# Performance work log

Measured on AMD Instinct MI355X. Metric: run time of the kernel, lower is better.

## Reference

```python
import jax, jax.numpy as jnp
import numpy as np

B, S, D = 4, 2048, 2048
H, HD = 16, 128  # n_heads, head_dim; H*HD == D


def setup_inputs() -> dict:
    key = jax.random.key(0)
    ks = jax.random.split(key, 9)
    inp = {
        "q": jax.random.normal(ks[0], (B, S, D), dtype=jnp.float32),
        "k": jax.random.normal(ks[1], (B, S, D), dtype=jnp.float32),
        "v": jax.random.normal(ks[2], (B, S, D), dtype=jnp.float32),
        "attention_mask": jax.random.normal(ks[3], (S, S), dtype=jnp.float32),
        "key_padding_mask": jnp.zeros((B, S), dtype=jnp.float32),
        # torch nn.Linear weights are [out_features, in_features], bias=False
        "wq": jax.random.normal(ks[4], (H * HD, D), dtype=jnp.float32) * (1.0 / np.sqrt(D)),
        "wk": jax.random.normal(ks[5], (H * HD, D), dtype=jnp.float32) * (1.0 / np.sqrt(D)),
        "wv": jax.random.normal(ks[6], (H * HD, D), dtype=jnp.float32) * (1.0 / np.sqrt(D)),
        "wo": jax.random.normal(ks[7], (D, H * HD), dtype=jnp.float32) * (1.0 / np.sqrt(H * HD)),
    }
    return inp


def reference(q, k, v, attention_mask, key_padding_mask, wq, wk, wv, wo):
    # projections: x @ W.T, then split into heads -> [B, H, S, HD]
    def proj_heads(x, w):
        y = jnp.einsum('bsd,ed->bse', x, w)
        return y.reshape(B, S, H, HD).transpose(0, 2, 1, 3)

    qh = proj_heads(q, wq)
    kh = proj_heads(k, wk)
    vh = proj_heads(v, wv)

    scale = 1.0 / jnp.sqrt(jnp.asarray(HD, dtype=qh.dtype))
    scores = jnp.einsum('bhqd,bhkd->bhqk', qh, kh) * scale  # [B,H,S,S]
    scores = scores + attention_mask[None, None, :, :]       # additive 2D mask
    scores = scores + key_padding_mask[:, None, None, :]     # additive padding mask
    weights = jax.nn.softmax(scores, axis=-1)
    attn = jnp.einsum('bhqk,bhkd->bhqd', weights, vh)        # [B,H,S,HD]

    combined = attn.transpose(0, 2, 1, 3).reshape(B, S, H * HD)
    out = jnp.einsum('bse,de->bsd', combined, wo)
    return out
```

## Files before the change

### kernel.cpp

```cpp
#include <hip/hip_runtime.h>
#include <hip/hip_bf16.h>
#include <stdint.h>

#define S_LEN 2048
#define D_MODEL 2048
#define NH 16
#define HD_DIM 128
#define BATCH 4

typedef unsigned short u16;
typedef unsigned int u32;
typedef short s16x8 __attribute__((ext_vector_type(8)));
typedef float f32x4 __attribute__((ext_vector_type(4)));

__device__ __forceinline__ u16 f2b(float f) {
    union { float f; u32 u; } v; v.f = f;
    u32 r = v.u + 0x7FFFu + ((v.u >> 16) & 1u);
    return (u16)(r >> 16);
}

__device__ __forceinline__ u32 cvtpk(float lo, float hi) {
    u32 r;
    asm("v_cvt_pk_bf16_f32 %0, %1, %2" : "=v"(r) : "v"(lo), "v"(hi));
    return r;
}

__device__ __forceinline__ float exp2a(float x) {
    float r;
    asm("v_exp_f32 %0, %1" : "=v"(r) : "v"(x));
    return r;
}
__device__ __forceinline__ float max3a(float a, float b, float c) {
    float r;
    asm("v_max3_f32 %0, %1, %2, %3" : "=v"(r) : "v"(a), "v"(b), "v"(c));
    return r;
}

#define L2E 1.4426950408889634f

#define BAR()   asm volatile("s_barrier" ::: "memory")
#define LGKM0() asm volatile("s_waitcnt lgkmcnt(0)" ::: "memory")
#define VMW(n)  asm volatile("s_waitcnt vmcnt(" #n ")" ::: "memory")

__global__ __launch_bounds__(256) void cvt_all(
    const float* __restrict__ wq, const float* __restrict__ wk,
    const float* __restrict__ wv, const float* __restrict__ wo,
    const float* __restrict__ q,  const float* __restrict__ k,
    const float* __restrict__ v,
    u16* __restrict__ wdst, u16* __restrict__ qdst,
    u16* __restrict__ kdst, u16* __restrict__ vdst) {
    int i = blockIdx.x * 256 + threadIdx.x;
    const float* src;
    u16* dst;
    if (i < 2097152) {
        const int seg = i >> 19, li = i & 524287;
        src = ((seg == 0) ? wq : (seg == 1) ? wk : (seg == 2) ? wv : wo) + (size_t)li * 8;
        dst = wdst + (size_t)i * 8;
    } else {
        const int j = i - 2097152;
        const int seg = j >> 21, li = j & 2097151;
        src = ((seg == 0) ? q : (seg == 1) ? k : v) + (size_t)li * 8;
        dst = ((seg == 0) ? qdst : (seg == 1) ? kdst : vdst) + (size_t)li * 8;
    }
    const float4* p = reinterpret_cast<const float4*>(src);
    float4 a = p[0], b = p[1];
    s16x8 o;
    o[0] = (short)f2b(a.x); o[1] = (short)f2b(a.y);
    o[2] = (short)f2b(a.z); o[3] = (short)f2b(a.w);
    o[4] = (short)f2b(b.x); o[5] = (short)f2b(b.y);
    o[6] = (short)f2b(b.z); o[7] = (short)f2b(b.w);
    *reinterpret_cast<s16x8*>(dst) = o;
}

template<int OUT_MODE>
__global__ __launch_bounds__(512, 1) void gemm256(const u16* __restrict__ Ab,
                                                  const u16* __restrict__ Bw,
                                                  void* __restrict__ Cv,
                                                  int M, int N, int K, float alpha) {
    __shared__ u16 lds[2][2][256 * 64];
    const int t = threadIdx.x, lane = t & 63, w = t >> 6;
    const int wm = w >> 2, wn = w & 3;
    const int lr = lane & 15, lk = lane >> 4;
    const int NT = K >> 6;

    const int ntile = N >> 8;
    int flat = blockIdx.x;
    int cpx = gridDim.x >> 3;
    int rmap = (flat & 7) * cpx + (flat >> 3);
    const int m0 = (rmap / ntile) * 256, n0 = (rmap % ntile) * 256;

    const int srow = t >> 3;
    const int spos = t & 7;
    const int scon = spos ^ (srow & 7);

    auto stage = [&](const u16* gbase, int grow0, int ldsT, int buf, int q, int kt) {
        const u16* src = gbase + (size_t)(grow0 + q * 64 + srow) * K + kt * 64 + scon * 8;
        u16* dst = &lds[buf][ldsT][(q * 64 + srow) * 64 + spos * 8];
        __builtin_amdgcn_global_load_lds(
            (const __attribute__((address_space(1))) void*)src,
            (__attribute__((address_space(3))) void*)dst, 16, 0, 0);
    };

    f32x4 acc[8][4];
#pragma unroll
    for (int i = 0; i < 8; ++i)
#pragma unroll
        for (int j = 0; j < 4; ++j) acc[i][j] = {0.f, 0.f, 0.f, 0.f};

    s16x8 a[4][2], b[4][2];

    stage(Bw, n0, 1, 0, 0, 0);
    stage(Bw, n0, 1, 0, 1, 0);
    stage(Bw, n0, 1, 0, 2, 0);
    stage(Bw, n0, 1, 0, 3, 0);
    stage(Ab, m0, 0, 0, 0, 0);
    stage(Ab, m0, 0, 0, 2, 0);
    stage(Ab, m0, 0, 0, 1, 0);
    stage(Ab, m0, 0, 0, 3, 0);
    VMW(2);
    BAR();

#define LDFRAG(base, row, kk) \
    (*(const s16x8*)((base) + (row) * 64 + ((((kk) * 4 + lk) ^ (lr & 7)) << 3)))

#define QUAD(mh, nh)                                                                   \
    __builtin_amdgcn_s_setprio(1);                                                     \
    _Pragma("unroll")                                                                  \
    for (int mf = 0; mf < 4; ++mf)                                                     \
        _Pragma("unroll")                                                              \
        for (int nf = 0; nf < 2; ++nf)                                                 \
            _Pragma("unroll")                                                          \
            for (int kk = 0; kk < 2; ++kk)                                             \
                acc[(mh) * 4 + mf][(nh) * 2 + nf] = __builtin_amdgcn_mfma_f32_16x16x32_bf16( \
                    a[mf][kk], b[(nh) * 2 + nf][kk], acc[(mh) * 4 + mf][(nh) * 2 + nf], 0, 0, 0); \
    __builtin_amdgcn_s_setprio(0);

    for (int kt = 0; kt < NT; ++kt) {
        const int buf = kt & 1;
        const u16* la = &lds[buf][0][0];
        const u16* lb = &lds[buf][1][0];
        const int nx = kt + 1;
        const bool st = nx < NT;

#pragma unroll
        for (int mf = 0; mf < 4; ++mf)
#pragma unroll
            for (int kk = 0; kk < 2; ++kk)
                a[mf][kk] = LDFRAG(la, wm * 128 + mf * 16 + lr, kk);
#pragma unroll
        for (int nf = 0; nf < 2; ++nf)
#pragma unroll
            for (int kk = 0; kk < 2; ++kk)
                b[nf][kk] = LDFRAG(lb, wn * 64 + nf * 16 + lr, kk);
        if (st) { stage(Bw, n0, 1, buf ^ 1, 0, nx); stage(Bw, n0, 1, buf ^ 1, 1, nx); }
        BAR();
        LGKM0();
        QUAD(0, 0);
        BAR();

#pragma unroll
        for (int nf = 2; nf < 4; ++nf)
#pragma unroll
            for (int kk = 0; kk < 2; ++kk)
                b[nf][kk] = LDFRAG(lb, wn * 64 + nf * 16 + lr, kk);
        if (st) { stage(Bw, n0, 1, buf ^ 1, 2, nx); stage(Bw, n0, 1, buf ^ 1, 3, nx); }
        BAR();
        LGKM0();
        QUAD(0, 1);
        if (kt == NT - 1) { VMW(0); } else { VMW(4); }
        BAR();

#pragma unroll
        for (int mf = 0; mf < 4; ++mf)
#pragma unroll
            for (int kk = 0; kk < 2; ++kk)
                a[mf][kk] = LDFRAG(la, wm * 128 + 64 + mf * 16 + lr, kk);
        if (st) { stage(Ab, m0, 0, buf ^ 1, 0, nx); stage(Ab, m0, 0, buf ^ 1, 2, nx); }
        BAR();
        LGKM0();
        QUAD(1, 0);
        BAR();

        if (st) { stage(Ab, m0, 0, buf ^ 1, 1, nx); stage(Ab, m0, 0, buf ^ 1, 3, nx); }
        BAR();
        QUAD(1, 1);
        VMW(2);
        BAR();
    }

#pragma unroll
    for (int i = 0; i < 8; ++i)
#pragma unroll
        for (int j = 0; j < 4; ++j) {
            int r0 = m0 + wm * 128 + (i >> 2) * 64 + (i & 3) * 16 + lk * 4;
            int c0 = n0 + wn * 64 + j * 16 + lr;
            if constexpr (OUT_MODE == 1) {
                float* C = (float*)Cv;
#pragma unroll
                for (int r = 0; r < 4; ++r) C[(size_t)(r0 + r) * N + c0] = acc[i][j][r] * alpha;
            } else {
                u16* C = (u16*)Cv;
#pragma unroll
                for (int r = 0; r < 4; ++r) C[(size_t)(r0 + r) * N + c0] = f2b(acc[i][j][r] * alpha);
            }
        }
}

__global__ __launch_bounds__(512, 2) void attn_kernel(
    const u16* __restrict__ Qh, const u16* __restrict__ Kh, const u16* __restrict__ Vh,
    const float* __restrict__ mask, const float* __restrict__ kpad,
    u16* __restrict__ Comb) {
    __shared__ u16 Ks[2][64 * 128];
    __shared__ u16 Vt[2][128 * 64];

    const int t = threadIdx.x, lane = t & 63, w = t >> 6;
    const int lr = lane & 15, lk = lane >> 4;

    const int g = blockIdx.x;
    const int rm = (g & 7) * 64 + (g >> 3);
    const int qb = rm & 7, h = (rm >> 3) & 15, b = rm >> 7;
    const int q0w = qb * 256 + w * 32;
    const size_t rowBase = (size_t)b * S_LEN;
    const u16* Kb = Kh + rowBase * D_MODEL + h * HD_DIM;
    const u16* Vb = Vh + rowBase * D_MODEL + h * HD_DIM;

    s16x8 qf[2][4];
#pragma unroll
    for (int qi = 0; qi < 2; ++qi)
#pragma unroll
        for (int dc = 0; dc < 4; ++dc)
            qf[qi][dc] = *(const s16x8*)(Qh + (rowBase + q0w + qi * 16 + lr) * D_MODEL +
                                         h * HD_DIM + dc * 32 + lk * 8);

    f32x4 o[2][8];
#pragma unroll
    for (int qi = 0; qi < 2; ++qi)
#pragma unroll
        for (int dt = 0; dt < 8; ++dt) o[qi][dt] = {0.f, 0.f, 0.f, 0.f};
    float m_[2] = {-3e38f, -3e38f}, l_[2] = {0.f, 0.f};

    const int ksub = t >> 4;
    const int kchunk = (t & 15) ^ (ksub & 7);
    const int vrow = t >> 3;
    const int vc0 = (t & 7) * 16;
    const int vodd = vrow & 1;
    const int vp = t >> 4;

    s16x8 va0, va1;

    auto stageK = [&](int kv0, int nb) {
#pragma unroll
        for (int p = 0; p < 2; ++p) {
            const u16* src = Kb + (size_t)(kv0 + p * 32 + ksub) * D_MODEL + kchunk * 8;
            __builtin_amdgcn_global_load_lds(
                (const __attribute__((address_space(1))) void*)src,
                (__attribute__((address_space(3))) void*)(&Ks[nb][p * 4096 + t * 8]), 16, 0, 0);
        }
    };
    auto loadV = [&](int kv0) {
        const u16* p0 = Vb + (size_t)(kv0 + vrow) * D_MODEL + vc0;
        va0 = *(const s16x8*)p0;
        va1 = *(const s16x8*)(p0 + 8);
    };
    auto writeV = [&](int nb) {
        union VU { s16x8 v[2]; u32 uw[8]; u16 us[16]; };
        VU A;
        A.v[0] = va0; A.v[1] = va1;
        u32 ra[4];
#pragma unroll
        for (int i = 0; i < 4; ++i)
            ra[i] = (u32)__shfl_xor((int)(vodd ? A.uw[i] : A.uw[i + 4]), 8, 64);
#pragma unroll
        for (int e = 0; e < 8; ++e) {
            int d = vc0 + vodd * 8 + e;
            int swz = ((d >> 4) ^ (d & 7)) & 7;
            u16 rau = (u16)((ra[e >> 1] >> ((e & 1) * 16)) & 0xffff);
            u16 lo1, hi1;
            if (vodd) { lo1 = rau; hi1 = A.us[8 + e]; }
            else      { lo1 = A.us[e]; hi1 = rau; }
            int c1 = (vp >> 2) ^ swz;
            *(u32*)(&Vt[nb][d * 64 + c1 * 8 + (vp & 3) * 2]) = (u32)lo1 | ((u32)hi1 << 16);
        }
    };

    f32x4 mreg[2][4], kreg[4];
    auto loadMask = [&](int kv0) {
#pragma unroll
        for (int qi = 0; qi < 2; ++qi) {
            const float* mrow = mask + (size_t)(q0w + qi * 16 + lr) * S_LEN + kv0;
#pragma unroll
            for (int kt = 0; kt < 4; ++kt)
                mreg[qi][kt] = *(const f32x4*)(mrow + kt * 16 + lk * 4);
        }
#pragma unroll
        for (int kt = 0; kt < 4; ++kt)
            kreg[kt] = *(const f32x4*)(kpad + b * S_LEN + kv0 + kt * 16 + lk * 4);
    };

    stageK(0, 0);
    loadV(0);
    writeV(0);
    loadMask(0);
    __syncthreads();

    const int srcA = ((lk & 1) * 32) + lr;
    const int srcB = srcA + 16;

    for (int i = 0; i < 32; ++i) {
        const int cur = i & 1;
        const u16* ks = &Ks[cur][0];
        const u16* vt = &Vt[cur][0];
        const int kv0 = i * 64;

        if (i < 31) { stageK(kv0 + 64, cur ^ 1); loadV(kv0 + 64); }

        f32x4 sc[2][4];
#pragma unroll
        for (int qi = 0; qi < 2; ++qi)
#pragma unroll
            for (int kt = 0; kt < 4; ++kt) sc[qi][kt] = {0.f, 0.f, 0.f, 0.f};
        __builtin_amdgcn_s_setprio(1);
#pragma unroll
        for (int kt = 0; kt < 4; ++kt) {
            s16x8 kf[4];
#pragma unroll
            for (int dc = 0; dc < 4; ++dc)
                kf[dc] = *(const s16x8*)(&ks[(kt * 16 + lr) * 128 +
                                             (((dc * 4 + lk) ^ (lr & 7)) << 3)]);
#pragma unroll
            for (int dc = 0; dc < 4; ++dc) {
                sc[0][kt] = __builtin_amdgcn_mfma_f32_16x16x32_bf16(kf[dc], qf[0][dc], sc[0][kt], 0, 0, 0);
                sc[1][kt] = __builtin_amdgcn_mfma_f32_16x16x32_bf16(kf[dc], qf[1][dc], sc[1][kt], 0, 0, 0);
            }
        }
        __builtin_amdgcn_s_setprio(0);

        u32 lo[2][4], hi[2][4];
#pragma unroll
        for (int qi = 0; qi < 2; ++qi) {
            float s[16];
#pragma unroll
            for (int kt = 0; kt < 4; ++kt)
#pragma unroll
                for (int r = 0; r < 4; ++r)
                    s[kt * 4 + r] = fmaf(mreg[qi][kt][r], L2E,
                                         fmaf(kreg[kt][r], L2E, sc[qi][kt][r]));
            float t0 = max3a(s[0], s[1], s[2]);
            float t1 = max3a(s[3], s[4], s[5]);
            float t2 = max3a(s[6], s[7], s[8]);
            float t3 = max3a(s[9], s[10], s[11]);
            float t4 = max3a(s[12], s[13], s[14]);
            float mx = fmaxf(max3a(t0, t1, t2), max3a(t3, t4, s[15]));
            mx = fmaxf(mx, __shfl_xor(mx, 16, 64));
            mx = fmaxf(mx, __shfl_xor(mx, 32, 64));
            if (__any(mx > m_[qi] + 11.5f)) {
                float mn = fmaxf(m_[qi], mx);
                float fs = exp2a(m_[qi] - mn);
                m_[qi] = mn;
                l_[qi] *= fs;
#pragma unroll
                for (int r = 0; r < 4; ++r) {
                    float fsb = __shfl(fs, (lane & 48) | (lk * 4 + r), 64);
#pragma unroll
                    for (int dt = 0; dt < 8; ++dt) o[qi][dt][r] *= fsb;
                }
            }
            float ls = 0.f;
#pragma unroll
            for (int e = 0; e < 16; ++e) { s[e] = exp2a(s[e] - m_[qi]); ls += s[e]; }
            ls += __shfl_xor(ls, 16, 64);
            ls += __shfl_xor(ls, 32, 64);
            l_[qi] += ls;
#pragma unroll
            for (int kt = 0; kt < 4; ++kt) {
                lo[qi][kt] = cvtpk(s[kt * 4 + 0], s[kt * 4 + 1]);
                hi[qi][kt] = cvtpk(s[kt * 4 + 2], s[kt * 4 + 3]);
            }
        }

        if (i < 31) loadMask(kv0 + 64);

        s16x8 pf[2][2];
        const bool sel = (lk >> 1) & 1;
#pragma unroll
        for (int qi = 0; qi < 2; ++qi)
#pragma unroll
            for (int hh = 0; hh < 2; ++hh) {
                u32 w0a = (u32)__shfl((int)lo[qi][2 * hh], srcA, 64);
                u32 w0b = (u32)__shfl((int)lo[qi][2 * hh + 1], srcA, 64);
                u32 w1a = (u32)__shfl((int)hi[qi][2 * hh], srcA, 64);
                u32 w1b = (u32)__shfl((int)hi[qi][2 * hh + 1], srcA, 64);
                u32 w2a = (u32)__shfl((int)lo[qi][2 * hh], srcB, 64);
                u32 w2b = (u32)__shfl((int)lo[qi][2 * hh + 1], srcB, 64);
                u32 w3a = (u32)__shfl((int)hi[qi][2 * hh], srcB, 64);
                u32 w3b = (u32)__shfl((int)hi[qi][2 * hh + 1], srcB, 64);
                union { s16x8 v; u32 u[4]; } P;
                P.u[0] = sel ? w0b : w0a;
                P.u[1] = sel ? w1b : w1a;
                P.u[2] = sel ? w2b : w2a;
                P.u[3] = sel ? w3b : w3a;
                pf[qi][hh] = P.v;
            }

        __builtin_amdgcn_s_setprio(1);
#pragma unroll
        for (int dt = 0; dt < 8; ++dt) {
            int swz = dt ^ (lr & 7);
            s16x8 vf0 = *(const s16x8*)(&vt[(dt * 16 + lr) * 64 + ((lk ^ swz) << 3)]);
            s16x8 vf1 = *(const s16x8*)(&vt[(dt * 16 + lr) * 64 + (((4 + lk) ^ swz) << 3)]);
            o[0][dt] = __builtin_amdgcn_mfma_f32_16x16x32_bf16(pf[0][0], vf0, o[0][dt], 0, 0, 0);
            o[1][dt] = __builtin_amdgcn_mfma_f32_16x16x32_bf16(pf[1][0], vf0, o[1][dt], 0, 0, 0);
            o[0][dt] = __builtin_amdgcn_mfma_f32_16x16x32_bf16(pf[0][1], vf1, o[0][dt], 0, 0, 0);
            o[1][dt] = __builtin_amdgcn_mfma_f32_16x16x32_bf16(pf[1][1], vf1, o[1][dt], 0, 0, 0);
        }
        __builtin_amdgcn_s_setprio(0);

        if (i < 31) writeV(cur ^ 1);
        LGKM0();
        BAR();
    }

#pragma unroll
    for (int qi = 0; qi < 2; ++qi)
#pragma unroll
        for (int r = 0; r < 4; ++r) {
            float lb = __shfl(l_[qi], (lane & 48) | (lk * 4 + r), 64);
            float inv = 1.0f / lb;
            size_t row = rowBase + q0w + qi * 16 + lk * 4 + r;
            u16* dst = Comb + row * D_MODEL + h * HD_DIM + lr;
#pragma unroll
            for (int dt = 0; dt < 8; ++dt) dst[dt * 16] = f2b(o[qi][dt][r] * inv);
        }
}

extern "C" void kernel_launch(void* const* d_in, const int* in_sizes, int n_in,
                              void* d_out, int out_size, void* d_ws, size_t ws_size,
                              hipStream_t stream) {
    const float* q    = (const float*)d_in[0];
    const float* k    = (const float*)d_in[1];
    const float* v    = (const float*)d_in[2];
    const float* mask = (const float*)d_in[3];
    const float* kpad = (const float*)d_in[4];
    const float* wq   = (const float*)d_in[5];
    const float* wk   = (const float*)d_in[6];
    const float* wv   = (const float*)d_in[7];
    const float* wo   = (const float*)d_in[8];
    float* out = (float*)d_out;

    u16* wqb  = (u16*)d_ws;
    u16* wkb  = wqb + 4194304;
    u16* wvb  = wkb + 4194304;
    u16* wob  = wvb + 4194304;
    u16* qh   = wob + 4194304;
    u16* kh   = qh + 16777216;
    u16* vh   = kh + 16777216;
    u16* comb = vh + 16777216;

    const float scale = 0.08838834764831845f * 1.4426950408889634f;

    {
        dim3 gc(8388608 / 256);
        cvt_all<<<gc, 256, 0, stream>>>(wq, wk, wv, wo, q, k, v, wqb, kh, vh, comb);
    }
    dim3 gg((8192 / 256) * (2048 / 256));

    gemm256<0><<<gg, 512, 0, stream>>>(kh,   wqb, qh, 8192, 2048, 2048, scale);
    gemm256<0><<<gg, 512, 0, stream>>>(vh,   wkb, kh, 8192, 2048, 2048, 1.0f);
    gemm256<0><<<gg, 512, 0, stream>>>(comb, wvb, vh, 8192, 2048, 2048, 1.0f);

    attn_kernel<<<dim3(512), 512, 0, stream>>>(qh, kh, vh, mask, kpad, comb);

    gemm256<1><<<gg, 512, 0, stream>>>(comb, wob, out, 8192, 2048, 2048, 1.0f);
}
```

Baseline: 567.8 us.

## Switch attention kernel to 32x32x16 MFMA tiles with transposed score layout

Rewrites the attention inner loop to use 32x32x16 bf16 MFMA instructions instead of 16x16x32. Each wave now computes its 32 query rows as a single 32-wide tile, which changes the register layouts for Q, scores and output. This reduces the cross-lane shuffles needed to rebuild P fragments for the PV product and the reductions for row max and row sum. The mask and padding tiles are now added together once per step ahead of time. The new lane mappings for mask, K/V LDS reads and output stores must match exactly, so correctness depends on that index arithmetic.

```diff
diff --git a/kernel.cpp b/kernel.cpp
--- a/kernel.cpp
+++ b/kernel.cpp
@@ -12,6 +12,7 @@
 typedef unsigned int u32;
 typedef short s16x8 __attribute__((ext_vector_type(8)));
 typedef float f32x4 __attribute__((ext_vector_type(4)));
+typedef float f32x16 __attribute__((ext_vector_type(16)));
 
 __device__ __forceinline__ u16 f2b(float f) {
     union { float f; u32 u; } v; v.f = f;
@@ -214,7 +215,7 @@
     __shared__ u16 Vt[2][128 * 64];
 
     const int t = threadIdx.x, lane = t & 63, w = t >> 6;
-    const int lr = lane & 15, lk = lane >> 4;
+    const int ln = lane & 31, hi = lane >> 5;
 
     const int g = blockIdx.x;
     const int rm = (g & 7) * 64 + (g >> 3);
@@ -224,20 +225,19 @@
     const u16* Kb = Kh + rowBase * D_MODEL + h * HD_DIM;
     const u16* Vb = Vh + rowBase * D_MODEL + h * HD_DIM;
 
-    s16x8 qf[2][4];
-#pragma unroll
-    for (int qi = 0; qi < 2; ++qi)
-#pragma unroll
-        for (int dc = 0; dc < 4; ++dc)
-            qf[qi][dc] = *(const s16x8*)(Qh + (rowBase + q0w + qi * 16 + lr) * D_MODEL +
-                                         h * HD_DIM + dc * 32 + lk * 8);
-
-    f32x4 o[2][8];
-#pragma unroll
-    for (int qi = 0; qi < 2; ++qi)
-#pragma unroll
-        for (int dt = 0; dt < 8; ++dt) o[qi][dt] = {0.f, 0.f, 0.f, 0.f};
-    float m_[2] = {-3e38f, -3e38f}, l_[2] = {0.f, 0.f};
+    s16x8 qf[8];
+    {
+        const u16* qp = Qh + (rowBase + q0w + ln) * D_MODEL + h * HD_DIM + hi * 8;
+#pragma unroll
+        for (int dsl = 0; dsl < 8; ++dsl) qf[dsl] = *(const s16x8*)(qp + dsl * 16);
+    }
+
+    f32x16 o[4];
+#pragma unroll
+    for (int dt = 0; dt < 4; ++dt)
+#pragma unroll
+        for (int r = 0; r < 16; ++r) o[dt][r] = 0.f;
+    float m_ = -3e38f, l_ = 0.f;
 
     const int ksub = t >> 4;
     const int kchunk = (t & 15) ^ (ksub & 7);
@@ -283,18 +283,24 @@
         }
     };
 
-    f32x4 mreg[2][4], kreg[4];
+    f32x4 mc[2][4];
+    f32x4 mt[2][4], kt_[2][4];
     auto loadMask = [&](int kv0) {
-#pragma unroll
-        for (int qi = 0; qi < 2; ++qi) {
-            const float* mrow = mask + (size_t)(q0w + qi * 16 + lr) * S_LEN + kv0;
-#pragma unroll
-            for (int kt = 0; kt < 4; ++kt)
-                mreg[qi][kt] = *(const f32x4*)(mrow + kt * 16 + lk * 4);
-        }
-#pragma unroll
-        for (int kt = 0; kt < 4; ++kt)
-            kreg[kt] = *(const f32x4*)(kpad + b * S_LEN + kv0 + kt * 16 + lk * 4);
+        const float* mrow = mask + (size_t)(q0w + ln) * S_LEN + kv0;
+        const float* krow = kpad + (size_t)b * S_LEN + kv0;
+#pragma unroll
+        for (int kk = 0; kk < 2; ++kk)
+#pragma unroll
+            for (int gg = 0; gg < 4; ++gg) {
+                mt[kk][gg] = *(const f32x4*)(mrow + kk * 32 + gg * 8 + hi * 4);
+                kt_[kk][gg] = *(const f32x4*)(krow + kk * 32 + gg * 8 + hi * 4);
+            }
+    };
+    auto combMask = [&]() {
+#pragma unroll
+        for (int kk = 0; kk < 2; ++kk)
+#pragma unroll
+            for (int gg = 0; gg < 4; ++gg) mc[kk][gg] = mt[kk][gg] + kt_[kk][gg];
     };
 
     stageK(0, 0);
@@ -302,9 +308,7 @@
     writeV(0);
     loadMask(0);
     __syncthreads();
-
-    const int srcA = ((lk & 1) * 32) + lr;
-    const int srcB = srcA + 16;
+    combMask();
 
     for (int i = 0; i < 32; ++i) {
         const int cur = i & 1;
@@ -314,123 +318,115 @@
 
         if (i < 31) { stageK(kv0 + 64, cur ^ 1); loadV(kv0 + 64); }
 
-        f32x4 sc[2][4];
-#pragma unroll
-        for (int qi = 0; qi < 2; ++qi)
-#pragma unroll
-            for (int kt = 0; kt < 4; ++kt) sc[qi][kt] = {0.f, 0.f, 0.f, 0.f};
+        f32x16 sc[2];
+#pragma unroll
+        for (int kk = 0; kk < 2; ++kk)
+#pragma unroll
+            for (int r = 0; r < 16; ++r) sc[kk][r] = 0.f;
         __builtin_amdgcn_s_setprio(1);
 #pragma unroll
-        for (int kt = 0; kt < 4; ++kt) {
-            s16x8 kf[4];
-#pragma unroll
-            for (int dc = 0; dc < 4; ++dc)
-                kf[dc] = *(const s16x8*)(&ks[(kt * 16 + lr) * 128 +
-                                             (((dc * 4 + lk) ^ (lr & 7)) << 3)]);
-#pragma unroll
-            for (int dc = 0; dc < 4; ++dc) {
-                sc[0][kt] = __builtin_amdgcn_mfma_f32_16x16x32_bf16(kf[dc], qf[0][dc], sc[0][kt], 0, 0, 0);
-                sc[1][kt] = __builtin_amdgcn_mfma_f32_16x16x32_bf16(kf[dc], qf[1][dc], sc[1][kt], 0, 0, 0);
+        for (int kk = 0; kk < 2; ++kk)
+#pragma unroll
+            for (int dsl = 0; dsl < 8; ++dsl) {
+                s16x8 kf = *(const s16x8*)(&ks[(kk * 32 + ln) * 128 +
+                                               (((dsl * 2 + hi) ^ (ln & 7)) << 3)]);
+                sc[kk] = __builtin_amdgcn_mfma_f32_32x32x16_bf16(kf, qf[dsl], sc[kk], 0, 0, 0);
+            }
+        __builtin_amdgcn_s_setprio(0);
+
+        float s[32];
+#pragma unroll
+        for (int kk = 0; kk < 2; ++kk)
+#pragma unroll
+            for (int r = 0; r < 16; ++r)
+                s[kk * 16 + r] = fmaf(mc[kk][r >> 2][r & 3], L2E, sc[kk][r]);
+
+        float t0 = max3a(s[0], s[1], s[2]);
+        float t1 = max3a(s[3], s[4], s[5]);
+        float t2 = max3a(s[6], s[7], s[8]);
+        float t3 = max3a(s[9], s[10], s[11]);
+        float t4 = max3a(s[12], s[13], s[14]);
+        float t5 = max3a(s[15], s[16], s[17]);
+        float t6 = max3a(s[18], s[19], s[20]);
+        float t7 = max3a(s[21], s[22], s[23]);
+        float t8 = max3a(s[24], s[25], s[26]);
+        float t9 = max3a(s[27], s[28], s[29]);
+        float ua = max3a(t0, t1, t2);
+        float ub = max3a(t3, t4, t5);
+        float uc = max3a(t6, t7, t8);
+        float ud = max3a(t9, s[30], s[31]);
+        float rmax = fmaxf(max3a(ua, ub, uc), ud);
+        rmax = fmaxf(rmax, __shfl_xor(rmax, 32, 64));
+
+        if (__any(rmax > m_ + 11.5f)) {
+            float mn = fmaxf(m_, rmax);
+            float fs = exp2a(m_ - mn);
+            m_ = mn;
+            l_ *= fs;
+#pragma unroll
+            for (int r = 0; r < 16; ++r) {
+                float fsb = __shfl(fs, (r & 3) + 8 * (r >> 2) + 4 * hi, 64);
+#pragma unroll
+                for (int dt = 0; dt < 4; ++dt) o[dt][r] *= fsb;
             }
         }
-        __builtin_amdgcn_s_setprio(0);
-
-        u32 lo[2][4], hi[2][4];
-#pragma unroll
-        for (int qi = 0; qi < 2; ++qi) {
-            float s[16];
-#pragma unroll
-            for (int kt = 0; kt < 4; ++kt)
-#pragma unroll
-                for (int r = 0; r < 4; ++r)
-                    s[kt * 4 + r] = fmaf(mreg[qi][kt][r], L2E,
-                                         fmaf(kreg[kt][r], L2E, sc[qi][kt][r]));
-            float t0 = max3a(s[0], s[1], s[2]);
-            float t1 = max3a(s[3], s[4], s[5]);
-            float t2 = max3a(s[6], s[7], s[8]);
-            float t3 = max3a(s[9], s[10], s[11]);
-            float t4 = max3a(s[12], s[13], s[14]);
-            float mx = fmaxf(max3a(t0, t1, t2), max3a(t3, t4, s[15]));
-            mx = fmaxf(mx, __shfl_xor(mx, 16, 64));
-            mx = fmaxf(mx, __shfl_xor(mx, 32, 64));
-            if (__any(mx > m_[qi] + 11.5f)) {
-                float mn = fmaxf(m_[qi], mx);
-                float fs = exp2a(m_[qi] - mn);
-                m_[qi] = mn;
-                l_[qi] *= fs;
-#pragma unroll
-                for (int r = 0; r < 4; ++r) {
-                    float fsb = __shfl(fs, (lane & 48) | (lk * 4 + r), 64);
-#pragma unroll
-                    for (int dt = 0; dt < 8; ++dt) o[qi][dt][r] *= fsb;
+
+        float ls = 0.f;
+#pragma unroll
+        for (int e = 0; e < 32; ++e) { s[e] = exp2a(s[e] - m_); ls += s[e]; }
+        ls += __shfl_xor(ls, 32, 64);
+        l_ += ls;
+
+        u32 wd[2][8];
+#pragma unroll
+        for (int kk = 0; kk < 2; ++kk)
+#pragma unroll
+            for (int p = 0; p < 8; ++p)
+                wd[kk][p] = cvtpk(s[kk * 16 + 2 * p], s[kk * 16 + 2 * p + 1]);
+
+        if (i < 31) loadMask(kv0 + 64);
+
+        __builtin_amdgcn_s_setprio(1);
+#pragma unroll
+        for (int kk = 0; kk < 2; ++kk)
+#pragma unroll
+            for (int sel = 0; sel < 2; ++sel) {
+                u32 pub0 = hi ? wd[kk][4 * sel + 0] : wd[kk][4 * sel + 2];
+                u32 pub1 = hi ? wd[kk][4 * sel + 1] : wd[kk][4 * sel + 3];
+                u32 r0 = (u32)__shfl_xor((int)pub0, 32, 64);
+                u32 r1 = (u32)__shfl_xor((int)pub1, 32, 64);
+                union { s16x8 v; u32 u[4]; } P;
+                P.u[0] = hi ? r0 : wd[kk][4 * sel + 0];
+                P.u[1] = hi ? r1 : wd[kk][4 * sel + 1];
+                P.u[2] = hi ? wd[kk][4 * sel + 2] : r0;
+                P.u[3] = hi ? wd[kk][4 * sel + 3] : r1;
+                const int ks4 = kk * 2 + sel;
+#pragma unroll
+                for (int dt = 0; dt < 4; ++dt) {
+                    int d = dt * 32 + ln;
+                    s16x8 vf = *(const s16x8*)(&vt[d * 64 +
+                                (((2 * ks4 + hi) ^ (((d >> 4) ^ d) & 7)) << 3)]);
+                    o[dt] = __builtin_amdgcn_mfma_f32_32x32x16_bf16(P.v, vf, o[dt], 0, 0, 0);
                 }
             }
-            float ls = 0.f;
-#pragma unroll
-            for (int e = 0; e < 16; ++e) { s[e] = exp2a(s[e] - m_[qi]); ls += s[e]; }
-            ls += __shfl_xor(ls, 16, 64);
-            ls += __shfl_xor(ls, 32, 64);
-            l_[qi] += ls;
-#pragma unroll
-            for (int kt = 0; kt < 4; ++kt) {
-                lo[qi][kt] = cvtpk(s[kt * 4 + 0], s[kt * 4 + 1]);
-                hi[qi][kt] = cvtpk(s[kt * 4 + 2], s[kt * 4 + 3]);
-            }
-        }
-
-        if (i < 31) loadMask(kv0 + 64);
-
-        s16x8 pf[2][2];
-        const bool sel = (lk >> 1) & 1;
-#pragma unroll
-        for (int qi = 0; qi < 2; ++qi)
-#pragma unroll
-            for (int hh = 0; hh < 2; ++hh) {
-                u32 w0a = (u32)__shfl((int)lo[qi][2 * hh], srcA, 64);
-                u32 w0b = (u32)__shfl((int)lo[qi][2 * hh + 1], srcA, 64);
-                u32 w1a = (u32)__shfl((int)hi[qi][2 * hh], srcA, 64);
-                u32 w1b = (u32)__shfl((int)hi[qi][2 * hh + 1], srcA, 64);
-                u32 w2a = (u32)__shfl((int)lo[qi][2 * hh], srcB, 64);
-                u32 w2b = (u32)__shfl((int)lo[qi][2 * hh + 1], srcB, 64);
-                u32 w3a = (u32)__shfl((int)hi[qi][2 * hh], srcB, 64);
-                u32 w3b = (u32)__shfl((int)hi[qi][2 * hh + 1], srcB, 64);
-                union { s16x8 v; u32 u[4]; } P;
-                P.u[0] = sel ? w0b : w0a;
-                P.u[1] = sel ? w1b : w1a;
-                P.u[2] = sel ? w2b : w2a;
-                P.u[3] = sel ? w3b : w3a;
-                pf[qi][hh] = P.v;
-            }
-
-        __builtin_amdgcn_s_setprio(1);
-#pragma unroll
-        for (int dt = 0; dt < 8; ++dt) {
-            int swz = dt ^ (lr & 7);
-            s16x8 vf0 = *(const s16x8*)(&vt[(dt * 16 + lr) * 64 + ((lk ^ swz) << 3)]);
-            s16x8 vf1 = *(const s16x8*)(&vt[(dt * 16 + lr) * 64 + (((4 + lk) ^ swz) << 3)]);
-            o[0][dt] = __builtin_amdgcn_mfma_f32_16x16x32_bf16(pf[0][0], vf0, o[0][dt], 0, 0, 0);
-            o[1][dt] = __builtin_amdgcn_mfma_f32_16x16x32_bf16(pf[1][0], vf0, o[1][dt], 0, 0, 0);
-            o[0][dt] = __builtin_amdgcn_mfma_f32_16x16x32_bf16(pf[0][1], vf1, o[0][dt], 0, 0, 0);
-            o[1][dt] = __builtin_amdgcn_mfma_f32_16x16x32_bf16(pf[1][1], vf1, o[1][dt], 0, 0, 0);
-        }
         __builtin_amdgcn_s_setprio(0);
 
         if (i < 31) writeV(cur ^ 1);
         LGKM0();
         BAR();
-    }
-
-#pragma unroll
-    for (int qi = 0; qi < 2; ++qi)
-#pragma unroll
-        for (int r = 0; r < 4; ++r) {
-            float lb = __shfl(l_[qi], (lane & 48) | (lk * 4 + r), 64);
-            float inv = 1.0f / lb;
-            size_t row = rowBase + q0w + qi * 16 + lk * 4 + r;
-            u16* dst = Comb + row * D_MODEL + h * HD_DIM + lr;
-#pragma unroll
-            for (int dt = 0; dt < 8; ++dt) dst[dt * 16] = f2b(o[qi][dt][r] * inv);
-        }
+        if (i < 31) combMask();
+    }
+
+    float inv = 1.0f / l_;
+#pragma unroll
+    for (int r = 0; r < 16; ++r) {
+        int qrow = (r & 3) + 8 * (r >> 2) + 4 * hi;
+        float invq = __shfl(inv, qrow, 64);
+        size_t row = rowBase + q0w + qrow;
+        u16* dst = Comb + row * D_MODEL + h * HD_DIM + ln;
+#pragma unroll
+        for (int dt = 0; dt < 4; ++dt) dst[dt * 32] = f2b(o[dt][r] * invq);
+    }
 }
 
 extern "C" void kernel_launch(void* const* d_in, const int* in_sizes, int n_in,
```

Result: slower. 582.0 us (+2.5%).
